# Kernel optimization log

Hardware: AMD Instinct MI355X
Metric: run time of the kernel (lower is better)

## Reference

```python
import jax, jax.numpy as jnp
import numpy as np
from jax.ops import segment_sum

N_NODES = 50000
N_EDGES = 800000
NUM_FEAT = 16
EDGE_DIM = 8
H = 100
L = 2
BN_EPS = 1e-5


def setup_inputs() -> dict:
    key = jax.random.key(0)
    ks = iter(jax.random.split(key, 40))
    def w(shape, scale=0.05):
        return (jax.random.normal(next(ks), shape, dtype=jnp.float32) * scale)
    inp = {
        "x": jax.random.normal(next(ks), (N_NODES, NUM_FEAT), dtype=jnp.float32),
        "edge_index": jax.random.randint(next(ks), (2, N_EDGES), 0, N_NODES, dtype=jnp.int64) if jax.config.jax_enable_x64 else jax.random.randint(next(ks), (2, N_EDGES), 0, N_NODES).astype(jnp.int32),
        "edge_attr": jax.random.normal(next(ks), (N_EDGES, EDGE_DIM), dtype=jnp.float32),
        # embeddings
        "node_w": w((NUM_FEAT, H)), "node_b": w((H,)),
        "edge_w": w((EDGE_DIM, H)), "edge_b": w((H,)),
        # per-layer GINEConv MLP (stacked over layers)
        "conv_w1": w((L, H, H)), "conv_b1": w((L, H)),
        "conv_w2": w((L, H, H)), "conv_b2": w((L, H)),
        # batchnorm affine params
        "bn_gamma": jnp.ones((L, H), dtype=jnp.float32), "bn_beta": jnp.zeros((L, H), dtype=jnp.float32),
        # per-layer edge-update MLP
        "emlp_w1": w((L, 3 * H, H)), "emlp_b1": w((L, H)),
        "emlp_w2": w((L, H, H)), "emlp_b2": w((L, H)),
        # final classifier MLP (3H -> 50 -> 25 -> 2); dropout is identity at eval
        "mlp_w1": w((3 * H, 50)), "mlp_b1": w((50,)),
        "mlp_w2": w((50, 25)), "mlp_b2": w((25,)),
        "mlp_w3": w((25, 2)), "mlp_b3": w((2,)),
    }
    return inp


def reference(x, edge_index, edge_attr,
              node_w, node_b, edge_w, edge_b,
              conv_w1, conv_b1, conv_w2, conv_b2,
              bn_gamma, bn_beta,
              emlp_w1, emlp_b1, emlp_w2, emlp_b2,
              mlp_w1, mlp_b1, mlp_w2, mlp_b2, mlp_w3, mlp_b3):
    src, dst = edge_index[0], edge_index[1]
    n_nodes = x.shape[0]

    h = x @ node_w + node_b          # [N, H]
    e = edge_attr @ edge_w + edge_b  # [E, H]

    for i in range(L):
        # GINEConv: out_i = nn((1+eps)*h_i + sum_{e: dst=i} relu(h_src + e)); eps=0
        msg = jax.nn.relu(h[src] + e)                       # [E, H] gather + combine
        agg = segment_sum(msg, dst, num_segments=n_nodes)   # [N, H] scatter-add
        z = h + agg
        z = jax.nn.relu(z @ conv_w1[i] + conv_b1[i]) @ conv_w2[i] + conv_b2[i]
        # BatchNorm (train mode: batch stats over nodes, biased variance)
        mu = jnp.mean(z, axis=0)
        var = jnp.var(z, axis=0)
        z = (z - mu) * jax.lax.rsqrt(var + BN_EPS) * bn_gamma[i] + bn_beta[i]
        h = (h + jax.nn.relu(z)) * 0.5
        # edge update: e += MLP([h_src, h_dst, e]) / 2
        cat = jnp.concatenate([h[src], h[dst], e], axis=-1)  # [E, 3H]
        upd = jax.nn.relu(cat @ emlp_w1[i] + emlp_b1[i]) @ emlp_w2[i] + emlp_b2[i]
        e = e + upd * 0.5

    # per-edge features: relu([h_src, h_dst]) ++ e  -> [E, 3H]
    feat = jnp.concatenate([jax.nn.relu(jnp.concatenate([h[src], h[dst]], axis=-1)), e], axis=-1)
    out = jax.nn.relu(feat @ mlp_w1 + mlp_b1)
    out = jax.nn.relu(out @ mlp_w2 + mlp_b2)
    return out @ mlp_w3 + mlp_b3  # [E, 2]
```

## Files before the change

kernel.cpp:

```cpp
#include <hip/hip_runtime.h>
#include <hip/hip_bf16.h>

#define N_NODES 50000
#define N_EDGES 800000
#define HDIM 100
#define ESTR 104

typedef _Float16 half8_t __attribute__((ext_vector_type(8)));
typedef _Float16 half4_t __attribute__((ext_vector_type(4)));
typedef float f32x4_t __attribute__((ext_vector_type(4)));

struct FragDesc {
  const float* src; int stride; int K; int N; int outOff; int ksteps; int ntiles;
};
struct PrepArgs {
  FragDesc d[20];
  int prefix[21];
  int ndesc;
};

__global__ void k_prep_frags(PrepArgs args, _Float16* __restrict__ out) {
  int b = blockIdx.x;
  int di = 0;
  while (di + 1 < args.ndesc && b >= args.prefix[di + 1]) di++;
  FragDesc d = args.d[di];
  int local = b - args.prefix[di];
  int t = local / d.ksteps;
  int s = local % d.ksteps;
  int lane = threadIdx.x;
  int col = t * 16 + (lane & 15);
  int kb = s * 32 + (lane >> 4) * 8;
  _Float16* o = out + d.outOff + (size_t)((t * d.ksteps + s) * 64 + lane) * 8;
  #pragma unroll
  for (int i = 0; i < 8; ++i) {
    int k = kb + i;
    float v = (k < d.K && col < d.N) ? d.src[(size_t)k * d.stride + col] : 0.0f;
    o[i] = (_Float16)v;
  }
}

__global__ void k_ws_probe(float* out, float mb) { out[0] = mb; }

__global__ void k_hist(const int* __restrict__ dst, int* __restrict__ cnt) {
  for (int e = blockIdx.x * blockDim.x + threadIdx.x; e < N_EDGES;
       e += gridDim.x * blockDim.x)
    atomicAdd(&cnt[dst[e]], 1);
}

__global__ __launch_bounds__(1024) void k_scan(const int* __restrict__ cnt,
                                               int* __restrict__ rowptr,
                                               int* __restrict__ cursor) {
  __shared__ int part[1024];
  int t = threadIdx.x;
  const int CH = (N_NODES + 1023) / 1024;
  int base = t * CH;
  int s = 0;
  for (int i = 0; i < CH; ++i) {
    int n = base + i;
    if (n < N_NODES) s += cnt[n];
  }
  part[t] = s;
  __syncthreads();
  for (int off = 1; off < 1024; off <<= 1) {
    int v = 0;
    if (t >= off) v = part[t - off];
    __syncthreads();
    if (t >= off) part[t] += v;
    __syncthreads();
  }
  int run = (t == 0) ? 0 : part[t - 1];
  for (int i = 0; i < CH; ++i) {
    int n = base + i;
    if (n <= N_NODES) {
      rowptr[n] = run;
      if (n < N_NODES) { cursor[n] = run; run += cnt[n]; }
    }
  }
}

__global__ void k_perm(const int* __restrict__ src, const int* __restrict__ dst,
                       int* __restrict__ cursor, int* __restrict__ perm,
                       int* __restrict__ srcS) {
  for (int e = blockIdx.x * blockDim.x + threadIdx.x; e < N_EDGES;
       e += gridDim.x * blockDim.x) {
    int pos = atomicAdd(&cursor[dst[e]], 1);
    perm[pos] = e;
    srcS[pos] = src[e];
  }
}

template<bool L0>
__global__ __launch_bounds__(256) void k_agg(
    const int* __restrict__ rowptr, const int* __restrict__ perm,
    const int* __restrict__ srcS,
    const float* __restrict__ attr, const float* __restrict__ ew,
    const float* __restrict__ ebias,
    const _Float16* __restrict__ e,
    const float* __restrict__ h, float* __restrict__ agg) {
  __shared__ float EwL[800];
  __shared__ float ebL[128];
  int tid = threadIdx.x;
  if constexpr (L0) {
    for (int idx = tid; idx < 800; idx += 256) EwL[idx] = ew[idx];
    if (tid < 128) ebL[tid] = (tid < HDIM) ? ebias[tid] : 0.0f;
    __syncthreads();
  }
  int n = blockIdx.x * 2 + (tid >> 7);
  int j = tid & 127;
  if (n >= N_NODES || j >= HDIM) return;
  float acc = 0.0f;
  int p0 = rowptr[n], p1 = rowptr[n + 1];
  for (int pos = p0; pos < p1; ++pos) {
    int s = srcS[pos];
    int eid = perm[pos];
    float m;
    if constexpr (L0) {
      const float* ap = attr + (size_t)eid * 8;
      float e0 = ebL[j];
      #pragma unroll
      for (int k = 0; k < 8; ++k) e0 += ap[k] * EwL[k * HDIM + j];
      m = h[(size_t)s * HDIM + j] + e0;
    } else {
      m = h[(size_t)s * HDIM + j] + (float)e[(size_t)eid * ESTR + j];
    }
    acc += fmaxf(m, 0.0f);
  }
  agg[(size_t)n * HDIM + j] = acc;
}

__device__ __forceinline__ half8_t h8_zero() {
  half8_t a;
  #pragma unroll
  for (int i = 0; i < 8; ++i) a[i] = (_Float16)0.0f;
  return a;
}

__device__ __forceinline__ int swz_idx(int r, int c) {
  int chunk = (c >> 3) ^ (r & 7);
  return r * 128 + chunk * 8 + (c & 7);
}

template<int MODE>
__device__ __forceinline__ void load_a_node(const float* hp0,
                                            const float* ap0,
                                            int row, int lane, half8_t av[4]) {
  int g = lane >> 4;
  bool rv = (row < N_NODES);
  const float* hp = hp0 + (size_t)row * HDIM;
  const float* ap = ap0 + (size_t)row * HDIM;
  #pragma unroll
  for (int s = 0; s < 4; ++s) {
    int kb = s * 32 + g * 8;
    half8_t a = h8_zero();
    if (rv && kb < HDIM) {
      float f[8];
      #pragma unroll
      for (int i = 0; i < 8; ++i) f[i] = 0.0f;
      if (kb + 8 <= HDIM) {
        float4 v0 = *(const float4*)(hp + kb);
        float4 v1 = *(const float4*)(hp + kb + 4);
        f[0] = v0.x; f[1] = v0.y; f[2] = v0.z; f[3] = v0.w;
        f[4] = v1.x; f[5] = v1.y; f[6] = v1.z; f[7] = v1.w;
        if constexpr (MODE == 2) {
          float4 u0 = *(const float4*)(ap + kb);
          float4 u1 = *(const float4*)(ap + kb + 4);
          f[0] += u0.x; f[1] += u0.y; f[2] += u0.z; f[3] += u0.w;
          f[4] += u1.x; f[5] += u1.y; f[6] += u1.z; f[7] += u1.w;
        }
      } else {
        float4 v0 = *(const float4*)(hp + kb);
        f[0] = v0.x; f[1] = v0.y; f[2] = v0.z; f[3] = v0.w;
        if constexpr (MODE == 2) {
          float4 u0 = *(const float4*)(ap + kb);
          f[0] += u0.x; f[1] += u0.y; f[2] += u0.z; f[3] += u0.w;
        }
      }
      #pragma unroll
      for (int i = 0; i < 8; ++i) {
        float v = f[i];
        if constexpr (MODE == 1) v = fmaxf(v, 0.0f);
        a[i] = (_Float16)v;
      }
    }
    av[s] = a;
  }
}

template<int NT, int KS>
__device__ __forceinline__ void mfma_tiles(const half8_t* av, const _Float16* __restrict__ fb,
                                           int lane, f32x4_t* acc) {
  #pragma unroll
  for (int t = 0; t < NT; ++t) {
    #pragma unroll
    for (int s = 0; s < KS; ++s) {
      half8_t bv = *(const half8_t*)(fb + (size_t)(((t * KS + s) * 64 + lane) << 3));
      acc[t] = __builtin_amdgcn_mfma_f32_16x16x32_f16(av[s], bv, acc[t], 0, 0, 0);
    }
  }
}

template<int KS>
__device__ __forceinline__ void lds_read_a(const _Float16* L, int lane, half8_t* av) {
  int r = lane & 15;
  int g = lane >> 4;
  #pragma unroll
  for (int s = 0; s < KS; ++s) {
    int kb = s * 32 + g * 8;
    av[s] = *(const half8_t*)&L[swz_idx(r, kb)];
  }
}

__global__ void k_embed_h(const float* __restrict__ x, const float* __restrict__ w,
                          const float* __restrict__ bias, float* __restrict__ h) {
  int n = blockIdx.x;
  int j = threadIdx.x;
  if (j >= HDIM) return;
  float acc = bias[j];
  #pragma unroll
  for (int k = 0; k < 16; ++k) acc += x[n * 16 + k] * w[k * HDIM + j];
  h[(size_t)n * HDIM + j] = acc;
}

__global__ void k_embed_e(const float* __restrict__ attr, const float* __restrict__ w,
                          const float* __restrict__ bias,
                          _Float16* __restrict__ e) {
  int tid = threadIdx.x;
  int edge = blockIdx.x * 2 + (tid >> 7);
  int j = tid & 127;
  if (edge >= N_EDGES || j >= ESTR) return;
  float acc = 0.0f;
  if (j < HDIM) {
    acc = bias[j];
    #pragma unroll
    for (int k = 0; k < 8; ++k) acc += attr[(size_t)edge * 8 + k] * w[k * HDIM + j];
  }
  e[(size_t)edge * ESTR + j] = (_Float16)acc;
}

__global__ __launch_bounds__(256) void k_node_conv(
    const float* __restrict__ h, const float* agg,
    const _Float16* __restrict__ fb1, const _Float16* __restrict__ fb2,
    const float* __restrict__ b1, const float* __restrict__ b2,
    float* z, float* __restrict__ bn_sum, float* __restrict__ bn_sq) {
  __shared__ __align__(16) _Float16 lds[4][2048];
  int lane = threadIdx.x & 63;
  int wave = threadIdx.x >> 6;
  _Float16* L = lds[wave];
  int mbase = (blockIdx.x * 4 + wave) * 16;

  half8_t av[4];
  load_a_node<2>(h, agg, mbase + (lane & 15), lane, av);
  f32x4_t acc[7];
  #pragma unroll
  for (int t = 0; t < 7; ++t) acc[t] = (f32x4_t){0.f, 0.f, 0.f, 0.f};
  mfma_tiles<7, 4>(av, fb1, lane, acc);

  #pragma unroll
  for (int t = 0; t < 7; ++t) {
    int j = t * 16 + (lane & 15);
    float bias = (j < HDIM) ? b1[j] : 0.0f;
    #pragma unroll
    for (int q = 0; q < 4; ++q) {
      int r = (lane >> 4) * 4 + q;
      float v = fmaxf(acc[t][q] + bias, 0.0f);
      if (j >= HDIM) v = 0.0f;
      L[swz_idx(r, j)] = (_Float16)v;
    }
  }
  {
    int r = lane >> 2; int c0 = 112 + (lane & 3) * 4;
    #pragma unroll
    for (int i = 0; i < 4; ++i) L[swz_idx(r, c0 + i)] = (_Float16)0.0f;
  }
  __builtin_amdgcn_sched_barrier(0);

  half8_t av2[4];
  lds_read_a<4>(L, lane, av2);
  f32x4_t acc2[7];
  #pragma unroll
  for (int t = 0; t < 7; ++t) acc2[t] = (f32x4_t){0.f, 0.f, 0.f, 0.f};
  mfma_tiles<7, 4>(av2, fb2, lane, acc2);
  __builtin_amdgcn_sched_barrier(0);

  #pragma unroll
  for (int t = 0; t < 7; ++t) {
    int j = t * 16 + (lane & 15);
    float bias = (j < HDIM) ? b2[j] : 0.0f;
    float colsum = 0.0f, colsq = 0.0f;
    #pragma unroll
    for (int q = 0; q < 4; ++q) {
      int row = mbase + (lane >> 4) * 4 + q;
      float v = acc2[t][q] + bias;
      bool ok = (row < N_NODES) && (j < HDIM);
      if (ok) z[(size_t)row * HDIM + j] = v;
      float sv = ok ? v : 0.0f;
      colsum += sv; colsq += sv * sv;
    }
    colsum += __shfl_xor(colsum, 16);
    colsum += __shfl_xor(colsum, 32);
    colsq  += __shfl_xor(colsq, 16);
    colsq  += __shfl_xor(colsq, 32);
    if (lane < 16 && j < HDIM) {
      atomicAdd(&bn_sum[j], colsum);
      atomicAdd(&bn_sq[j], colsq);
    }
  }
}

__global__ void k_bn_final(const float* __restrict__ bn_sum, const float* __restrict__ bn_sq,
                           float* __restrict__ bn_mu, float* __restrict__ bn_rs) {
  int j = threadIdx.x;
  if (j >= HDIM) return;
  float mu = bn_sum[j] / (float)N_NODES;
  float var = bn_sq[j] / (float)N_NODES - mu * mu;
  bn_mu[j] = mu;
  bn_rs[j] = rsqrtf(var + 1e-5f);
}

__global__ void k_h_update(float* __restrict__ h, const float* __restrict__ z,
                           const float* __restrict__ bn_mu, const float* __restrict__ bn_rs,
                           const float* __restrict__ gamma, const float* __restrict__ beta) {
  int idx = blockIdx.x * blockDim.x + threadIdx.x;
  if (idx >= N_NODES * HDIM) return;
  int j = idx % HDIM;
  float zn = (z[idx] - bn_mu[j]) * bn_rs[j] * gamma[j] + beta[j];
  h[idx] = 0.5f * (h[idx] + fmaxf(zn, 0.0f));
}

template<bool RS>
__global__ __launch_bounds__(256) void k_node_gemm_t(const float* __restrict__ h,
                                                     const _Float16* __restrict__ fb,
                                                     _Float16* __restrict__ out) {
  constexpr int NT = RS ? 8 : 14;
  int lane = threadIdx.x & 63;
  int wave = threadIdx.x >> 6;
  int c = lane & 15;
  int mbase = (blockIdx.x * 4 + wave) * 16;
  half8_t av[4];
  load_a_node<RS ? 1 : 0>(h, h, mbase + c, lane, av);
  f32x4_t acc[NT];
  #pragma unroll
  for (int t = 0; t < NT; ++t) acc[t] = (f32x4_t){0.f, 0.f, 0.f, 0.f};
  mfma_tiles<NT, 4>(av, fb, lane, acc);
  #pragma unroll
  for (int q = 0; q < 4; ++q) {
    int row = mbase + (lane >> 4) * 4 + q;
    if (row >= N_NODES) continue;
    if constexpr (!RS) {
      half8_t hp, hq;
      #pragma unroll
      for (int t = 0; t < 8; ++t) {
        hp[t] = (t < 7) ? (_Float16)acc[t][q] : (_Float16)0.0f;
        hq[t] = (t < 7) ? (_Float16)acc[7 + t][q] : (_Float16)0.0f;
      }
      *(half8_t*)(out + (size_t)row * 256 + c * 8) = hp;
      *(half8_t*)(out + (size_t)row * 256 + 128 + c * 8) = hq;
    } else {
      half4_t hr, hs;
      #pragma unroll
      for (int t = 0; t < 4; ++t) {
        hr[t] = (_Float16)acc[t][q];
        hs[t] = (_Float16)acc[4 + t][q];
      }
      *(half4_t*)(out + (size_t)row * 128 + c * 4) = hr;
      *(half4_t*)(out + (size_t)row * 128 + 64 + c * 4) = hs;
    }
  }
}

template<bool CLASSIFY>
__global__ __launch_bounds__(256) void k_edge(
    _Float16* __restrict__ e,
    const _Float16* __restrict__ PQ,
    const int* __restrict__ src, const int* __restrict__ dst,
    const _Float16* __restrict__ fbW1c, const _Float16* __restrict__ fbW2,
    const float* __restrict__ b1, const float* __restrict__ b2,
    const _Float16* __restrict__ RS,
    const _Float16* __restrict__ fbC, const _Float16* __restrict__ fbM2,
    const _Float16* __restrict__ fbM3,
    const float* __restrict__ mb1, const float* __restrict__ mb2,
    const float* __restrict__ mb3,
    float* __restrict__ out) {
  __shared__ __align__(16) _Float16 lds[4][2048];
  int lane = threadIdx.x & 63;
  int wave = threadIdx.x >> 6;
  _Float16* L = lds[wave];
  int mbase = (blockIdx.x * 4 + wave) * 16;
  int c = lane & 15, g = lane >> 4;

  int sn[4], dn[4];
  #pragma unroll
  for (int q = 0; q < 4; ++q) {
    int row = mbase + g * 4 + q;
    sn[q] = src[row]; dn[q] = dst[row];
  }

  half8_t Pf[4], Qf[4];
  #pragma unroll
  for (int q = 0; q < 4; ++q) {
    Pf[q] = *(const half8_t*)(PQ + (size_t)sn[q] * 256 + c * 8);
    Qf[q] = *(const half8_t*)(PQ + (size_t)dn[q] * 256 + 128 + c * 8);
  }

  half8_t av[4];
  {
    const _Float16* ep = e + (size_t)(mbase + c) * ESTR;
    #pragma unroll
    for (int s = 0; s < 3; ++s)
      av[s] = *(const half8_t*)(ep + s * 32 + g * 8);
    av[3] = (g == 0) ? *(const half8_t*)(ep + 96) : h8_zero();
  }
  f32x4_t acc[7];
  #pragma unroll
  for (int t = 0; t < 7; ++t) acc[t] = (f32x4_t){0.f, 0.f, 0.f, 0.f};
  mfma_tiles<7, 4>(av, fbW1c, lane, acc);

  #pragma unroll
  for (int t = 0; t < 7; ++t) {
    int j = t * 16 + c;
    float bias = (j < HDIM) ? b1[j] : 0.0f;
    #pragma unroll
    for (int q = 0; q < 4; ++q) {
      int r = g * 4 + q;
      float v = 0.0f;
      if (j < HDIM)
        v = fmaxf(acc[t][q] + bias + (float)Pf[q][t] + (float)Qf[q][t], 0.0f);
      L[swz_idx(r, j)] = (_Float16)v;
    }
  }
  { int r = lane >> 2; int c0 = 112 + (lane & 3) * 4;
    #pragma unroll
    for (int i = 0; i < 4; ++i) L[swz_idx(r, c0 + i)] = (_Float16)0.0f;
  }
  __builtin_amdgcn_sched_barrier(0);

  half4_t Rf[4], Sf[4];
  if constexpr (CLASSIFY) {
    #pragma unroll
    for (int q = 0; q < 4; ++q) {
      Rf[q] = *(const half4_t*)(RS + (size_t)sn[q] * 128 + c * 4);
      Sf[q] = *(const half4_t*)(RS + (size_t)dn[q] * 128 + 64 + c * 4);
    }
  }

  half8_t av2[4];
  lds_read_a<4>(L, lane, av2);
  f32x4_t acc2[7];
  #pragma unroll
  for (int t = 0; t < 7; ++t) acc2[t] = (f32x4_t){0.f, 0.f, 0.f, 0.f};
  mfma_tiles<7, 4>(av2, fbW2, lane, acc2);
  __builtin_amdgcn_sched_barrier(0);

  #pragma unroll
  for (int t = 0; t < 7; ++t) {
    int j = t * 16 + c;
    float bias = (j < HDIM) ? b2[j] : 0.0f;
    #pragma unroll
    for (int q = 0; q < 4; ++q) {
      int row = mbase + g * 4 + q;
      float upd = acc2[t][q] + bias;
      float enew = 0.0f;
      if (j < HDIM) {
        float eold = (float)e[(size_t)row * ESTR + j];
        enew = eold + 0.5f * upd;
      }
      if constexpr (!CLASSIFY) {
        if (j < HDIM) e[(size_t)row * ESTR + j] = (_Float16)enew;
      } else {
        int r = g * 4 + q;
        L[swz_idx(r, j)] = (_Float16)((j < HDIM) ? enew : 0.0f);
      }
    }
  }

  if constexpr (CLASSIFY) {
    __builtin_amdgcn_sched_barrier(0);
    half8_t av3[4];
    lds_read_a<4>(L, lane, av3);
    f32x4_t acc3[4];
    #pragma unroll
    for (int t = 0; t < 4; ++t) acc3[t] = (f32x4_t){0.f, 0.f, 0.f, 0.f};
    mfma_tiles<4, 4>(av3, fbC, lane, acc3);
    __builtin_amdgcn_sched_barrier(0);
    #pragma unroll
    for (int t = 0; t < 4; ++t) {
      int j = t * 16 + c;
      float bias = (j < 50) ? mb1[j] : 0.0f;
      #pragma unroll
      for (int q = 0; q < 4; ++q) {
        float v = 0.0f;
        if (j < 50)
          v = fmaxf(acc3[t][q] + bias + (float)Rf[q][t] + (float)Sf[q][t], 0.0f);
        int r = g * 4 + q;
        L[swz_idx(r, j)] = (_Float16)v;
      }
    }
    __builtin_amdgcn_sched_barrier(0);
    half8_t av4[2];
    lds_read_a<2>(L, lane, av4);
    f32x4_t acc4[2];
    #pragma unroll
    for (int t = 0; t < 2; ++t) acc4[t] = (f32x4_t){0.f, 0.f, 0.f, 0.f};
    mfma_tiles<2, 2>(av4, fbM2, lane, acc4);
    __builtin_amdgcn_sched_barrier(0);
    #pragma unroll
    for (int t = 0; t < 2; ++t) {
      int j = t * 16 + c;
      float bias = (j < 25) ? mb2[j] : 0.0f;
      #pragma unroll
      for (int q = 0; q < 4; ++q) {
        float v = (j < 25) ? fmaxf(acc4[t][q] + bias, 0.0f) : 0.0f;
        int r = g * 4 + q;
        L[swz_idx(r, j)] = (_Float16)v;
      }
    }
    __builtin_amdgcn_sched_barrier(0);
    half8_t av5[1];
    lds_read_a<1>(L, lane, av5);
    f32x4_t acc5 = (f32x4_t){0.f, 0.f, 0.f, 0.f};
    {
      half8_t bv = *(const half8_t*)(fbM3 + (size_t)(lane << 3));
      acc5 = __builtin_amdgcn_mfma_f32_16x16x32_f16(av5[0], bv, acc5, 0, 0, 0);
    }
    if (c < 2) {
      float bias = mb3[c];
      #pragma unroll
      for (int q = 0; q < 4; ++q) {
        int row = mbase + g * 4 + q;
        out[(size_t)row * 2 + c] = acc5[q] + bias;
      }
    }
  }
}

extern "C" void kernel_launch(void* const* d_in, const int* in_sizes, int n_in,
                              void* d_out, int out_size, void* d_ws, size_t ws_size,
                              hipStream_t stream) {
  const float* x        = (const float*)d_in[0];
  const int*   ei       = (const int*)  d_in[1];
  const float* eattr    = (const float*)d_in[2];
  const float* node_w   = (const float*)d_in[3];
  const float* node_b   = (const float*)d_in[4];
  const float* edge_w   = (const float*)d_in[5];
  const float* edge_b   = (const float*)d_in[6];
  const float* conv_w1  = (const float*)d_in[7];
  const float* conv_b1  = (const float*)d_in[8];
  const float* conv_w2  = (const float*)d_in[9];
  const float* conv_b2  = (const float*)d_in[10];
  const float* bn_gamma = (const float*)d_in[11];
  const float* bn_beta  = (const float*)d_in[12];
  const float* emlp_w1  = (const float*)d_in[13];
  const float* emlp_b1  = (const float*)d_in[14];
  const float* emlp_w2  = (const float*)d_in[15];
  const float* emlp_b2  = (const float*)d_in[16];
  const float* mlp_w1   = (const float*)d_in[17];
  const float* mlp_b1   = (const float*)d_in[18];
  const float* mlp_w2   = (const float*)d_in[19];
  const float* mlp_b2   = (const float*)d_in[20];
  const float* mlp_w3   = (const float*)d_in[21];
  const float* mlp_b3   = (const float*)d_in[22];
  const int* src = ei;
  const int* dst = ei + N_EDGES;

  char* ws = (char*)d_ws;
  size_t off = 0;
  auto alloc = [&](size_t bytes) -> void* {
    void* p = ws + off;
    off += (bytes + 255) & ~(size_t)255;
    return p;
  };
  _Float16* e    = (_Float16*)alloc((size_t)N_EDGES * ESTR * 2);
  float* h       = (float*)alloc((size_t)N_NODES * HDIM * 4);
  float* agg     = (float*)alloc((size_t)N_NODES * HDIM * 4);
  _Float16* PQt  = (_Float16*)alloc((size_t)N_NODES * 256 * 2);
  int* cnt       = (int*)alloc((size_t)N_NODES * 4);
  int* cursor    = (int*)alloc((size_t)N_NODES * 4);
  int* rowptr    = (int*)alloc((size_t)(N_NODES + 1) * 4);
  int* perm      = (int*)alloc((size_t)N_EDGES * 4);
  int* srcS      = (int*)alloc((size_t)N_EDGES * 4);
  float* bn_sum  = (float*)alloc(512);
  float* bn_sq   = (float*)alloc(512);
  float* bn_mu   = (float*)alloc(512);
  float* bn_rs   = (float*)alloc(512);
  _Float16* frags = (_Float16*)alloc(200000 * 2);
  float* z = agg;
  _Float16* RSt = (_Float16*)agg;

  if (off > ws_size) {
    k_ws_probe<<<1, 1, 0, stream>>>((float*)d_out, (float)(ws_size >> 20));
    return;
  }

  PrepArgs pa;
  int nd = 0, tilesum = 0, fo = 0;
  auto add = [&](const float* sp, int stride, int K, int Ncols, int ksteps, int ntiles) -> int {
    pa.d[nd] = FragDesc{sp, stride, K, Ncols, fo, ksteps, ntiles};
    pa.prefix[nd] = tilesum;
    tilesum += ksteps * ntiles;
    ++nd;
    int ret = fo;
    fo += ksteps * ntiles * 512;
    return ret;
  };
  int offConvW1[2], offConvW2[2], offPQ[2], offW1c[2], offW2e[2];
  for (int i = 0; i < 2; ++i) {
    offConvW1[i] = add(conv_w1 + i * 10000, 100, 100, 100, 4, 7);
    offConvW2[i] = add(conv_w2 + i * 10000, 100, 100, 100, 4, 7);
    offPQ[i]     = add(emlp_w1 + i * 30000,         100, 100, 100, 4, 7);
                   add(emlp_w1 + i * 30000 + 10000, 100, 100, 100, 4, 7);
    offW1c[i]    = add(emlp_w1 + i * 30000 + 20000, 100, 100, 100, 4, 7);
    offW2e[i]    = add(emlp_w2 + i * 10000, 100, 100, 100, 4, 7);
  }
  int offRS = add(mlp_w1,         50, 100, 50, 4, 4);
              add(mlp_w1 + 5000,  50, 100, 50, 4, 4);
  int offC  = add(mlp_w1 + 10000, 50, 100, 50, 4, 4);
  int offM2 = add(mlp_w2, 25, 50, 25, 2, 2);
  int offM3 = add(mlp_w3, 2, 25, 2, 1, 1);
  pa.prefix[nd] = tilesum;
  pa.ndesc = nd;

  hipMemsetAsync(cnt, 0, (size_t)N_NODES * 4, stream);
  k_hist<<<2048, 256, 0, stream>>>(dst, cnt);
  k_scan<<<1, 1024, 0, stream>>>(cnt, rowptr, cursor);
  k_perm<<<2048, 256, 0, stream>>>(src, dst, cursor, perm, srcS);

  k_prep_frags<<<tilesum, 64, 0, stream>>>(pa, frags);
  k_embed_h<<<N_NODES, 128, 0, stream>>>(x, node_w, node_b, h);
  k_embed_e<<<N_EDGES / 2, 256, 0, stream>>>(eattr, edge_w, edge_b, e);
  k_agg<true><<<N_NODES / 2, 256, 0, stream>>>(rowptr, perm, srcS,
                                               eattr, edge_w, edge_b,
                                               nullptr, h, agg);

  const int nodeGrid = (N_NODES + 63) / 64;
  for (int i = 0; i < 2; ++i) {
    hipMemsetAsync(bn_sum, 0, 512, stream);
    hipMemsetAsync(bn_sq, 0, 512, stream);
    k_node_conv<<<nodeGrid, 256, 0, stream>>>(h, agg, frags + offConvW1[i], frags + offConvW2[i],
                                              conv_b1 + i * 100, conv_b2 + i * 100,
                                              z, bn_sum, bn_sq);
    k_bn_final<<<1, 128, 0, stream>>>(bn_sum, bn_sq, bn_mu, bn_rs);
    k_h_update<<<(N_NODES * HDIM + 255) / 256, 256, 0, stream>>>(h, z, bn_mu, bn_rs,
                                                                 bn_gamma + i * 100, bn_beta + i * 100);
    k_node_gemm_t<false><<<nodeGrid, 256, 0, stream>>>(h, frags + offPQ[i], PQt);
    if (i == 0) {
      k_edge<false><<<N_EDGES / 64, 256, 0, stream>>>(
          e, PQt, src, dst, frags + offW1c[0], frags + offW2e[0],
          emlp_b1, emlp_b2,
          nullptr, nullptr, nullptr, nullptr, nullptr, nullptr, nullptr, nullptr);
      k_agg<false><<<N_NODES / 2, 256, 0, stream>>>(rowptr, perm, srcS,
                                                    nullptr, nullptr, nullptr,
                                                    e, h, agg);
    } else {
      k_node_gemm_t<true><<<nodeGrid, 256, 0, stream>>>(h, frags + offRS, RSt);
      k_edge<true><<<N_EDGES / 64, 256, 0, stream>>>(
          e, PQt, src, dst, frags + offW1c[1], frags + offW2e[1],
          emlp_b1 + 100, emlp_b2 + 100,
          RSt, frags + offC, frags + offM2, frags + offM3,
          mlp_b1, mlp_b2, mlp_b3, (float*)d_out);
    }
  }
}
```

Baseline: 1.658 ms.

## Fuse edge embedding into first edge-update kernel and reuse staged e via LDS

Removes the standalone edge-embedding kernel and computes the initial edge features inside the layer-0 edge kernel from edge_attr, using edge weights staged in shared memory. This avoids writing the fp16 e buffer once and reading it back twice in layer 0. The layer-1 classify kernel now stages the already-loaded e tile through LDS to get the residual values, instead of re-reading e from global memory. The cost is extra per-block weight loading and a small per-edge FMA loop of scalar ALU work in k_edge0, plus more register and LDS pressure.

```diff
diff --git a/kernel.cpp b/kernel.cpp
--- a/kernel.cpp
+++ b/kernel.cpp
@@ -221,22 +221,6 @@
   h[(size_t)n * HDIM + j] = acc;
 }
 
-__global__ void k_embed_e(const float* __restrict__ attr, const float* __restrict__ w,
-                          const float* __restrict__ bias,
-                          _Float16* __restrict__ e) {
-  int tid = threadIdx.x;
-  int edge = blockIdx.x * 2 + (tid >> 7);
-  int j = tid & 127;
-  if (edge >= N_EDGES || j >= ESTR) return;
-  float acc = 0.0f;
-  if (j < HDIM) {
-    acc = bias[j];
-    #pragma unroll
-    for (int k = 0; k < 8; ++k) acc += attr[(size_t)edge * 8 + k] * w[k * HDIM + j];
-  }
-  e[(size_t)edge * ESTR + j] = (_Float16)acc;
-}
-
 __global__ __launch_bounds__(256) void k_node_conv(
     const float* __restrict__ h, const float* agg,
     const _Float16* __restrict__ fb1, const _Float16* __restrict__ fb2,
@@ -368,19 +352,130 @@
   }
 }
 
-template<bool CLASSIFY>
-__global__ __launch_bounds__(256) void k_edge(
-    _Float16* __restrict__ e,
+__global__ __launch_bounds__(256) void k_edge0(
+    const float* __restrict__ attr,
     const _Float16* __restrict__ PQ,
+    const int* __restrict__ src, const int* __restrict__ dst,
+    const float* __restrict__ ew, const float* __restrict__ ebias,
+    const _Float16* __restrict__ fbW1c, const _Float16* __restrict__ fbW2,
+    const float* __restrict__ b1, const float* __restrict__ b2,
+    _Float16* __restrict__ e) {
+  __shared__ __align__(16) _Float16 lds[4][2048];
+  __shared__ float EwL[800];
+  __shared__ float ebL[112];
+  int tid = threadIdx.x;
+  for (int idx = tid; idx < 800; idx += 256) EwL[idx] = ew[idx];
+  if (tid < 112) ebL[tid] = (tid < HDIM) ? ebias[tid] : 0.0f;
+  __syncthreads();
+
+  int lane = tid & 63;
+  int wave = tid >> 6;
+  _Float16* L = lds[wave];
+  int mbase = (blockIdx.x * 4 + wave) * 16;
+  int c = lane & 15, g = lane >> 4;
+
+  int sn[4], dn[4];
+  #pragma unroll
+  for (int q = 0; q < 4; ++q) {
+    int row = mbase + g * 4 + q;
+    sn[q] = src[row]; dn[q] = dst[row];
+  }
+
+  half8_t Pf[4], Qf[4];
+  #pragma unroll
+  for (int q = 0; q < 4; ++q) {
+    Pf[q] = *(const half8_t*)(PQ + (size_t)sn[q] * 256 + c * 8);
+    Qf[q] = *(const half8_t*)(PQ + (size_t)dn[q] * 256 + 128 + c * 8);
+  }
+
+  float af[4][8];
+  #pragma unroll
+  for (int q = 0; q < 4; ++q) {
+    const float* ap = attr + (size_t)(mbase + g * 4 + q) * 8;
+    float4 a0 = *(const float4*)ap;
+    float4 a1 = *(const float4*)(ap + 4);
+    af[q][0] = a0.x; af[q][1] = a0.y; af[q][2] = a0.z; af[q][3] = a0.w;
+    af[q][4] = a1.x; af[q][5] = a1.y; af[q][6] = a1.z; af[q][7] = a1.w;
+  }
+
+  float e0r[7][4];
+  #pragma unroll
+  for (int t = 0; t < 7; ++t) {
+    int j = t * 16 + c;
+    #pragma unroll
+    for (int q = 0; q < 4; ++q) {
+      float v = 0.0f;
+      if (j < HDIM) {
+        v = ebL[j];
+        #pragma unroll
+        for (int k = 0; k < 8; ++k) v += af[q][k] * EwL[k * HDIM + j];
+      }
+      e0r[t][q] = v;
+      L[swz_idx(g * 4 + q, j)] = (_Float16)v;
+    }
+  }
+  { int r = lane >> 2; int c0 = 112 + (lane & 3) * 4;
+    #pragma unroll
+    for (int i = 0; i < 4; ++i) L[swz_idx(r, c0 + i)] = (_Float16)0.0f;
+  }
+  __builtin_amdgcn_sched_barrier(0);
+
+  half8_t av[4];
+  lds_read_a<4>(L, lane, av);
+  __builtin_amdgcn_sched_barrier(0);
+  f32x4_t acc[7];
+  #pragma unroll
+  for (int t = 0; t < 7; ++t) acc[t] = (f32x4_t){0.f, 0.f, 0.f, 0.f};
+  mfma_tiles<7, 4>(av, fbW1c, lane, acc);
+
+  #pragma unroll
+  for (int t = 0; t < 7; ++t) {
+    int j = t * 16 + c;
+    float bias = (j < HDIM) ? b1[j] : 0.0f;
+    #pragma unroll
+    for (int q = 0; q < 4; ++q) {
+      int r = g * 4 + q;
+      float v = 0.0f;
+      if (j < HDIM)
+        v = fmaxf(acc[t][q] + bias + (float)Pf[q][t] + (float)Qf[q][t], 0.0f);
+      L[swz_idx(r, j)] = (_Float16)v;
+    }
+  }
+  __builtin_amdgcn_sched_barrier(0);
+
+  half8_t av2[4];
+  lds_read_a<4>(L, lane, av2);
+  f32x4_t acc2[7];
+  #pragma unroll
+  for (int t = 0; t < 7; ++t) acc2[t] = (f32x4_t){0.f, 0.f, 0.f, 0.f};
+  mfma_tiles<7, 4>(av2, fbW2, lane, acc2);
+  __builtin_amdgcn_sched_barrier(0);
+
+  #pragma unroll
+  for (int t = 0; t < 7; ++t) {
+    int j = t * 16 + c;
+    float b2v = (j < HDIM) ? b2[j] : 0.0f;
+    #pragma unroll
+    for (int q = 0; q < 4; ++q) {
+      int row = mbase + g * 4 + q;
+      float eold = (float)(_Float16)e0r[t][q];
+      float enew = eold + 0.5f * (acc2[t][q] + b2v);
+      if (j < ESTR)
+        e[(size_t)row * ESTR + j] = (j < HDIM) ? (_Float16)enew : (_Float16)0.0f;
+    }
+  }
+}
+
+__global__ __launch_bounds__(256) void k_edge1(
+    const _Float16* __restrict__ e,
+    const _Float16* __restrict__ PQ, const _Float16* __restrict__ RS,
     const int* __restrict__ src, const int* __restrict__ dst,
     const _Float16* __restrict__ fbW1c, const _Float16* __restrict__ fbW2,
     const float* __restrict__ b1, const float* __restrict__ b2,
-    const _Float16* __restrict__ RS,
     const _Float16* __restrict__ fbC, const _Float16* __restrict__ fbM2,
     const _Float16* __restrict__ fbM3,
     const float* __restrict__ mb1, const float* __restrict__ mb2,
-    const float* __restrict__ mb3,
-    float* __restrict__ out) {
+    const float* __restrict__ mb3, float* __restrict__ out) {
   __shared__ __align__(16) _Float16 lds[4][2048];
   int lane = threadIdx.x & 63;
   int wave = threadIdx.x >> 6;
@@ -410,6 +505,18 @@
       av[s] = *(const half8_t*)(ep + s * 32 + g * 8);
     av[3] = (g == 0) ? *(const half8_t*)(ep + 96) : h8_zero();
   }
+  #pragma unroll
+  for (int s = 0; s < 4; ++s)
+    *(half8_t*)&L[swz_idx(c, s * 32 + g * 8)] = av[s];
+  __builtin_amdgcn_sched_barrier(0);
+  _Float16 eoldv[7][4];
+  #pragma unroll
+  for (int t = 0; t < 7; ++t)
+    #pragma unroll
+    for (int q = 0; q < 4; ++q)
+      eoldv[t][q] = L[swz_idx(g * 4 + q, t * 16 + c)];
+  __builtin_amdgcn_sched_barrier(0);
+
   f32x4_t acc[7];
   #pragma unroll
   for (int t = 0; t < 7; ++t) acc[t] = (f32x4_t){0.f, 0.f, 0.f, 0.f};
@@ -435,12 +542,10 @@
   __builtin_amdgcn_sched_barrier(0);
 
   half4_t Rf[4], Sf[4];
-  if constexpr (CLASSIFY) {
-    #pragma unroll
-    for (int q = 0; q < 4; ++q) {
-      Rf[q] = *(const half4_t*)(RS + (size_t)sn[q] * 128 + c * 4);
-      Sf[q] = *(const half4_t*)(RS + (size_t)dn[q] * 128 + 64 + c * 4);
-    }
+  #pragma unroll
+  for (int q = 0; q < 4; ++q) {
+    Rf[q] = *(const half4_t*)(RS + (size_t)sn[q] * 128 + c * 4);
+    Sf[q] = *(const half4_t*)(RS + (size_t)dn[q] * 128 + 64 + c * 4);
   }
 
   half8_t av2[4];
@@ -457,78 +562,68 @@
     float bias = (j < HDIM) ? b2[j] : 0.0f;
     #pragma unroll
     for (int q = 0; q < 4; ++q) {
+      float v = 0.0f;
+      if (j < HDIM)
+        v = (float)eoldv[t][q] + 0.5f * (acc2[t][q] + bias);
+      int r = g * 4 + q;
+      L[swz_idx(r, j)] = (_Float16)v;
+    }
+  }
+  __builtin_amdgcn_sched_barrier(0);
+
+  half8_t av3[4];
+  lds_read_a<4>(L, lane, av3);
+  f32x4_t acc3[4];
+  #pragma unroll
+  for (int t = 0; t < 4; ++t) acc3[t] = (f32x4_t){0.f, 0.f, 0.f, 0.f};
+  mfma_tiles<4, 4>(av3, fbC, lane, acc3);
+  __builtin_amdgcn_sched_barrier(0);
+  #pragma unroll
+  for (int t = 0; t < 4; ++t) {
+    int j = t * 16 + c;
+    float bias = (j < 50) ? mb1[j] : 0.0f;
+    #pragma unroll
+    for (int q = 0; q < 4; ++q) {
+      float v = 0.0f;
+      if (j < 50)
+        v = fmaxf(acc3[t][q] + bias + (float)Rf[q][t] + (float)Sf[q][t], 0.0f);
+      int r = g * 4 + q;
+      L[swz_idx(r, j)] = (_Float16)v;
+    }
+  }
+  __builtin_amdgcn_sched_barrier(0);
+  half8_t av4[2];
+  lds_read_a<2>(L, lane, av4);
+  f32x4_t acc4[2];
+  #pragma unroll
+  for (int t = 0; t < 2; ++t) acc4[t] = (f32x4_t){0.f, 0.f, 0.f, 0.f};
+  mfma_tiles<2, 2>(av4, fbM2, lane, acc4);
+  __builtin_amdgcn_sched_barrier(0);
+  #pragma unroll
+  for (int t = 0; t < 2; ++t) {
+    int j = t * 16 + c;
+    float bias = (j < 25) ? mb2[j] : 0.0f;
+    #pragma unroll
+    for (int q = 0; q < 4; ++q) {
+      float v = (j < 25) ? fmaxf(acc4[t][q] + bias, 0.0f) : 0.0f;
+      int r = g * 4 + q;
+      L[swz_idx(r, j)] = (_Float16)v;
+    }
+  }
+  __builtin_amdgcn_sched_barrier(0);
+  half8_t av5[1];
+  lds_read_a<1>(L, lane, av5);
+  f32x4_t acc5 = (f32x4_t){0.f, 0.f, 0.f, 0.f};
+  {
+    half8_t bv = *(const half8_t*)(fbM3 + (size_t)(lane << 3));
+    acc5 = __builtin_amdgcn_mfma_f32_16x16x32_f16(av5[0], bv, acc5, 0, 0, 0);
+  }
+  if (c < 2) {
+    float bias = mb3[c];
+    #pragma unroll
+    for (int q = 0; q < 4; ++q) {
       int row = mbase + g * 4 + q;
-      float upd = acc2[t][q] + bias;
-      float enew = 0.0f;
-      if (j < HDIM) {
-        float eold = (float)e[(size_t)row * ESTR + j];
-        enew = eold + 0.5f * upd;
-      }
-      if constexpr (!CLASSIFY) {
-        if (j < HDIM) e[(size_t)row * ESTR + j] = (_Float16)enew;
-      } else {
-        int r = g * 4 + q;
-        L[swz_idx(r, j)] = (_Float16)((j < HDIM) ? enew : 0.0f);
-      }
-    }
-  }
-
-  if constexpr (CLASSIFY) {
-    __builtin_amdgcn_sched_barrier(0);
-    half8_t av3[4];
-    lds_read_a<4>(L, lane, av3);
-    f32x4_t acc3[4];
-    #pragma unroll
-    for (int t = 0; t < 4; ++t) acc3[t] = (f32x4_t){0.f, 0.f, 0.f, 0.f};
-    mfma_tiles<4, 4>(av3, fbC, lane, acc3);
-    __builtin_amdgcn_sched_barrier(0);
-    #pragma unroll
-    for (int t = 0; t < 4; ++t) {
-      int j = t * 16 + c;
-      float bias = (j < 50) ? mb1[j] : 0.0f;
-      #pragma unroll
-      for (int q = 0; q < 4; ++q) {
-        float v = 0.0f;
-        if (j < 50)
-          v = fmaxf(acc3[t][q] + bias + (float)Rf[q][t] + (float)Sf[q][t], 0.0f);
-        int r = g * 4 + q;
-        L[swz_idx(r, j)] = (_Float16)v;
-      }
-    }
-    __builtin_amdgcn_sched_barrier(0);
-    half8_t av4[2];
-    lds_read_a<2>(L, lane, av4);
-    f32x4_t acc4[2];
-    #pragma unroll
-    for (int t = 0; t < 2; ++t) acc4[t] = (f32x4_t){0.f, 0.f, 0.f, 0.f};
-    mfma_tiles<2, 2>(av4, fbM2, lane, acc4);
-    __builtin_amdgcn_sched_barrier(0);
-    #pragma unroll
-    for (int t = 0; t < 2; ++t) {
-      int j = t * 16 + c;
-      float bias = (j < 25) ? mb2[j] : 0.0f;
-      #pragma unroll
-      for (int q = 0; q < 4; ++q) {
-        float v = (j < 25) ? fmaxf(acc4[t][q] + bias, 0.0f) : 0.0f;
-        int r = g * 4 + q;
-        L[swz_idx(r, j)] = (_Float16)v;
-      }
-    }
-    __builtin_amdgcn_sched_barrier(0);
-    half8_t av5[1];
-    lds_read_a<1>(L, lane, av5);
-    f32x4_t acc5 = (f32x4_t){0.f, 0.f, 0.f, 0.f};
-    {
-      half8_t bv = *(const half8_t*)(fbM3 + (size_t)(lane << 3));
-      acc5 = __builtin_amdgcn_mfma_f32_16x16x32_f16(av5[0], bv, acc5, 0, 0, 0);
-    }
-    if (c < 2) {
-      float bias = mb3[c];
-      #pragma unroll
-      for (int q = 0; q < 4; ++q) {
-        int row = mbase + g * 4 + q;
-        out[(size_t)row * 2 + c] = acc5[q] + bias;
-      }
+      out[(size_t)row * 2 + c] = acc5[q] + bias;
     }
   }
 }
@@ -626,7 +721,6 @@
 
   k_prep_frags<<<tilesum, 64, 0, stream>>>(pa, frags);
   k_embed_h<<<N_NODES, 128, 0, stream>>>(x, node_w, node_b, h);
-  k_embed_e<<<N_EDGES / 2, 256, 0, stream>>>(eattr, edge_w, edge_b, e);
   k_agg<true><<<N_NODES / 2, 256, 0, stream>>>(rowptr, perm, srcS,
                                                eattr, edge_w, edge_b,
                                                nullptr, h, agg);
@@ -643,19 +737,20 @@
                                                                  bn_gamma + i * 100, bn_beta + i * 100);
     k_node_gemm_t<false><<<nodeGrid, 256, 0, stream>>>(h, frags + offPQ[i], PQt);
     if (i == 0) {
-      k_edge<false><<<N_EDGES / 64, 256, 0, stream>>>(
-          e, PQt, src, dst, frags + offW1c[0], frags + offW2e[0],
-          emlp_b1, emlp_b2,
-          nullptr, nullptr, nullptr, nullptr, nullptr, nullptr, nullptr, nullptr);
+      k_edge0<<<N_EDGES / 64, 256, 0, stream>>>(
+          eattr, PQt, src, dst, edge_w, edge_b,
+          frags + offW1c[0], frags + offW2e[0],
+          emlp_b1, emlp_b2, e);
       k_agg<false><<<N_NODES / 2, 256, 0, stream>>>(rowptr, perm, srcS,
                                                     nullptr, nullptr, nullptr,
                                                     e, h, agg);
     } else {
       k_node_gemm_t<true><<<nodeGrid, 256, 0, stream>>>(h, frags + offRS, RSt);
-      k_edge<true><<<N_EDGES / 64, 256, 0, stream>>>(
-          e, PQt, src, dst, frags + offW1c[1], frags + offW2e[1],
+      k_edge1<<<N_EDGES / 64, 256, 0, stream>>>(
+          e, PQt, RSt, src, dst,
+          frags + offW1c[1], frags + offW2e[1],
           emlp_b1 + 100, emlp_b2 + 100,
-          RSt, frags + offC, frags + offM2, frags + offM3,
+          frags + offC, frags + offM2, frags + offM3,
           mlp_b1, mlp_b2, mlp_b3, (float*)d_out);
     }
   }
```

Result: faster. 1.596 ms (-3.8%).
